# Kernel tuning notes

Measured on AMD Instinct MI355X. Metric: run time of the kernel, lower is better.

## Reference

```python
import jax, jax.numpy as jnp
from jax import lax
import numpy as np

RNN = 512; FC = 512; COND = 128; FEAT = 80; NCLS = 256; HALF = RNN // 2
PAD = 2; SCALES = (5, 5, 11); MEL_T = 86  # -> 22550 output samples


def setup_inputs() -> dict:
    key = jax.random.key(0)
    ks = jax.random.split(key, 12)
    s = 0.05
    p = {"mels": jax.random.normal(ks[0], (1, FEAT, MEL_T), jnp.float32)}
    ch = FEAT
    for i, sc in enumerate(SCALES):
        k = 2 * sc + 1
        p[f"up_w{i}"] = jax.random.normal(ks[1 + i], (COND, ch, k), jnp.float32) * s
        p[f"up_b{i}"] = jnp.zeros((COND,), jnp.float32)
        ch = COND
    p["Wx"] = jax.random.normal(ks[4], (3 * RNN, 3 + COND), jnp.float32) * s
    p["bx"] = jnp.zeros((3 * RNN,), jnp.float32)
    p["Wh"] = jax.random.normal(ks[5], (3 * RNN, RNN), jnp.float32) * s
    p["bh"] = jnp.zeros((3 * RNN,), jnp.float32)
    p["O1w"] = jax.random.normal(ks[6], (FC, HALF), jnp.float32) * s
    p["O1b"] = jnp.zeros((FC,), jnp.float32)
    p["O2w"] = jax.random.normal(ks[7], (NCLS, FC), jnp.float32) * s
    p["O2b"] = jnp.zeros((NCLS,), jnp.float32)
    p["O3w"] = jax.random.normal(ks[8], (FC, HALF), jnp.float32) * s
    p["O3b"] = jnp.zeros((FC,), jnp.float32)
    p["O4w"] = jax.random.normal(ks[9], (NCLS, FC), jnp.float32) * s
    p["O4b"] = jnp.zeros((NCLS,), jnp.float32)
    return p


def _upsample(mels, ws, bs):
    # mels[:, :, excess_pad:-excess_pad] with excess_pad = PAD - 1 = 1
    x = mels[:, :, PAD - 1:-(PAD - 1)]
    for w, b, sc in zip(ws, bs, SCALES):
        k = 2 * sc + 1
        # ConvTranspose1d(stride=sc, kernel=k, padding=(3*sc-1)//2) as an
        # input-dilated conv: edge pad = k-1-torch_pad = (sc+1)//2
        e = k - 1 - (3 * sc - 1) // 2
        x = lax.conv_general_dilated(x, w, window_strides=(1,),
                                     padding=[(e, e)], lhs_dilation=(sc,),
                                     dimension_numbers=('NCH', 'OIH', 'NCH'))
        x = jax.nn.relu(x + b[None, :, None])
    return x[0, :, 1:-1].T  # [T, COND]


def _gru(inp, h, Wx, bx, Wh, bh):
    xg = Wx @ inp + bx
    hg = Wh @ h + bh
    xr, xz, xn = jnp.split(xg, 3)
    hr, hz, hn = jnp.split(hg, 3)
    r = jax.nn.sigmoid(xr + hr)
    z = jax.nn.sigmoid(xz + hz)
    n = jnp.tanh(xn + r * hn)
    return (1.0 - z) * n + z * h


def reference(mels, up_w0, up_b0, up_w1, up_b1, up_w2, up_b2,
              Wx, bx, Wh, bh, O1w, O1b, O2w, O2b, O3w, O3b, O4w, O4b):
    cond = _upsample(mels, (up_w0, up_w1, up_w2), (up_b0, up_b1, up_b2))
    zero = jnp.float32(0.0)

    def step(carry, m_t):
        h, c_val, f_val = carry
        # coarse pass: x = [c_{t-1}, f_{t-1}, 0]
        inp1 = jnp.concatenate([jnp.stack([c_val, f_val, zero]), m_t])
        h1 = _gru(inp1, h, Wx, bx, Wh, bh)
        oc = O2w @ jax.nn.relu(O1w @ h1[:HALF] + O1b) + O2b
        c_cat = jnp.argmax(oc).astype(jnp.float32)  # deterministic=True path
        c_new = c_cat / 127.5 - 1.0
        # fine pass: x = [c_{t-1}, f_{t-1}, c_t]
        inp2 = jnp.concatenate([jnp.stack([c_val, f_val, c_new]), m_t])
        h2 = _gru(inp2, h, Wx, bx, Wh, bh)
        of = O4w @ jax.nn.relu(O3w @ h2[HALF:] + O3b) + O4b
        f_cat = jnp.argmax(of).astype(jnp.float32)
        f_new = f_cat / 127.5 - 1.0
        sample = (c_cat * 256.0 + f_cat) / 32767.5 - 1.0
        return (h2, c_new, f_new), (sample, jnp.concatenate([oc, of]))

    init = (jnp.zeros((RNN,), jnp.float32), zero, zero)
    _, (samples, logits) = lax.scan(step, init, cond)
    return samples, logits  # [T], [T, 512]
```

## Files before the change

### kernel.cpp

```cpp
#include <hip/hip_runtime.h>
#include <math.h>

#define T_STEPS 22550
#define NWG 32
#define NTHR 256

typedef unsigned long long ull;

#define SL_PRE  0
#define SL_PLC  2048
#define SL_PLF  10240
#define SL_END  18432

#define OF_SLOT  64
#define OF_AFTER (OF_SLOT + SL_END*2)
#define OF_BUFA  OF_AFTER
#define OF_BUFB  (OF_BUFA + 128*412)
#define OF_COND  (OF_BUFB + 128*2052)

__global__ void k_init(float* ws){
  int i = blockIdx.x*blockDim.x + threadIdx.x;
  ull* sl = (ull*)(ws + OF_SLOT);
  if (i < SL_END) __hip_atomic_store(&sl[i], 0ULL, __ATOMIC_RELAXED, __HIP_MEMORY_SCOPE_AGENT);
}

__global__ void k_upconv(const float* __restrict__ x, int instride, int inoff,
                         const float* __restrict__ w, const float* __restrict__ b,
                         float* __restrict__ y, int Cin, int Lin, int K, int sc, int e,
                         int Lout, int mode)
{
  int j = blockIdx.x*blockDim.x + threadIdx.x;
  int c = blockIdx.y;
  if (j >= Lout) return;
  float acc = b[c];
  int kstart = ((e - j) % sc + sc) % sc;
  for (int i = 0; i < Cin; ++i){
    const float* wci = w + (c*Cin + i)*K;
    const float* xi  = x + i*instride + inoff;
    for (int k = kstart; k < K; k += sc){
      int qd = j - e + k;
      if (qd >= 0){
        int qq = qd / sc;
        if (qq < Lin) acc += wci[k]*xi[qq];
      }
    }
  }
  acc = fmaxf(acc, 0.f);
  if (mode == 0) y[c*Lout + j] = acc;
  else { int t = j - 1; if (t >= 0 && t < T_STEPS) y[t*128 + c] = acc; }
}

__device__ __forceinline__ float sigm(float x){ return 1.f/(1.f + expf(-x)); }

__device__ __forceinline__ void pub64(ull* p, ull pk){
  (void)__hip_atomic_exchange(p, pk, __ATOMIC_RELAXED, __HIP_MEMORY_SCOPE_AGENT);
}
__device__ __forceinline__ ull ld64(ull* p){
  return __hip_atomic_load(p, __ATOMIC_RELAXED, __HIP_MEMORY_SCOPE_AGENT);
}
__device__ __forceinline__ ull pack_data(float v, unsigned tag){
  return ((ull)__float_as_uint(v) << 32) | (ull)tag;
}

__launch_bounds__(NTHR)
__global__ void k_wavernn(const float* __restrict__ Wx, const float* __restrict__ bx,
                          const float* __restrict__ Wh, const float* __restrict__ bh,
                          const float* __restrict__ O1w, const float* __restrict__ O1b,
                          const float* __restrict__ O2w, const float* __restrict__ O2b,
                          const float* __restrict__ O3w, const float* __restrict__ O3b,
                          const float* __restrict__ O4w, const float* __restrict__ O4b,
                          float* ws, float* __restrict__ out)
{
  __shared__ __align__(16) float h_s[512];
  __shared__ __align__(16) float m_s[128];
  __shared__ __align__(16) float h1_s[256];
  __shared__ __align__(16) float logit_s[256];
  __shared__ __align__(16) float pr_s[512], pz_s[512], pna_s[512], hn_s[512];
  __shared__ __align__(16) float w1r_s[512], w1z_s[512], w1n_s[512];
  __shared__ __align__(16) float w2r_s[512], w2z_s[512], w2n_s[512];
  __shared__ float o1own_s[16], o3own_s[16];
  __shared__ float hg_s[48], xgb_s[48];
  __shared__ float sc_s[8];
  __shared__ float wc0_s[48], bx_s[48], bh_s[48];

  const int tid = threadIdx.x, g = blockIdx.x;
  ull* sl = (ull*)(ws + OF_SLOT);
  const float* cond = ws + OF_COND;
  float* out_samp = out;
  float* out_log  = out + T_STEPS;

  if (tid < 48){
    int row = (tid>>4)*512 + g + 32*(tid&15);
    wc0_s[tid] = Wx[(size_t)row*131 + 0];
    bx_s[tid]  = bx[row];
    bh_s[tid]  = bh[row];
  }
  for (int e = tid; e < 512; e += NTHR){
    w1r_s[e] = Wx[(size_t)e*131 + 1];
    w1z_s[e] = Wx[(size_t)(512+e)*131 + 1];
    w1n_s[e] = Wx[(size_t)(1024+e)*131 + 1];
    w2r_s[e] = Wx[(size_t)e*131 + 2];
    w2z_s[e] = Wx[(size_t)(512+e)*131 + 2];
    w2n_s[e] = Wx[(size_t)(1024+e)*131 + 2];
  }
  const int m16 = tid>>4, c16 = tid&15;
  const int rowO1 = g + 32*m16;
  float wO1r[16], wO3r[16];
  #pragma unroll
  for (int k=0;k<16;++k){
    wO1r[k] = O1w[(size_t)rowO1*256 + c16*16 + k];
    wO3r[k] = O3w[(size_t)rowO1*256 + c16*16 + k];
  }
  const float bO1r = O1b[rowO1], bO3r = O3b[rowO1];
  float wPC[16], wPF[16];
  #pragma unroll
  for (int m=0;m<16;++m){
    wPC[m] = O2w[(size_t)tid*512 + g + 32*m];
    wPF[m] = O4w[(size_t)tid*512 + g + 32*m];
  }
  const float cbO2 = O2b[tid], cbO4 = O4b[tid];

  h_s[tid] = 0.f; h_s[tid+256] = 0.f;
  if (tid < 128) m_s[tid] = cond[tid];
  if (tid == 0){ sc_s[0] = 0.f; sc_s[2] = 0.f; sc_s[3] = 0.f; }
  __syncthreads();

  #define COMPUTE_WX() do { \
    if (tid < 192){ \
      const int li_ = tid>>2, q_ = tid&3; \
      const int row_ = (li_>>4)*512 + g + 32*(li_&15); \
      const float* WxR = Wx + (size_t)row_*131 + 3; \
      float aX = 0.f; \
      _Pragma("unroll") \
      for (int kk=0; kk<32; ++kk){ \
        int f_ = q_*32 + ((kk + 8*q_) & 31); \
        aX += WxR[f_]*m_s[f_]; \
      } \
      aX += __shfl_xor(aX,1); aX += __shfl_xor(aX,2); \
      if (q_ == 0) xgb_s[li_] = aX + bx_s[li_]; \
    } } while(0)

  #define COMPUTE_WH() do { \
    if (tid < 192){ \
      const int li_ = tid>>2, q_ = tid&3; \
      const int row_ = (li_>>4)*512 + g + 32*(li_&15); \
      const float4* W4 = (const float4*)(Wh + (size_t)row_*512); \
      const float4* H4 = (const float4*)h_s; \
      float aH = 0.f; \
      _Pragma("unroll") \
      for (int kk=0; kk<32; ++kk){ \
        int f_ = q_*32 + ((kk + 2*q_) & 31); \
        float4 w = W4[f_], v = H4[f_]; \
        aH += w.x*v.x + w.y*v.y + w.z*v.z + w.w*v.w; \
      } \
      aH += __shfl_xor(aH,1); aH += __shfl_xor(aH,2); \
      if (q_ == 0) hg_s[li_] = aH + bh_s[li_]; \
    } } while(0)

  #define PUB_PREGATES(TAGP) do { \
    if (tid < 64){ \
      const int i_ = tid>>2, c_ = tid&3; \
      const int e_ = g + 32*i_; \
      const float c0_ = sc_s[3]; \
      float v_; \
      if (c_ == 0)      v_ = xgb_s[i_]    + c0_*wc0_s[i_]    + hg_s[i_]; \
      else if (c_ == 1) v_ = xgb_s[16+i_] + c0_*wc0_s[16+i_] + hg_s[16+i_]; \
      else if (c_ == 2) v_ = xgb_s[32+i_] + c0_*wc0_s[32+i_]; \
      else              v_ = hg_s[32+i_]; \
      pub64(&sl[SL_PRE + e_*4 + c_], pack_data(v_, (TAGP))); \
    } } while(0)

  #define FAT_GATHER(BASE, BIAS) do { \
    ull pk_[32]; \
    _Pragma("unroll") \
    for (int g2=0; g2<32; ++g2) pk_[g2] = ld64(&sl[(BASE) + g2*256 + tid]); \
    for (;;){ \
      bool all_ = true; \
      _Pragma("unroll") \
      for (int g2=0; g2<32; ++g2) if ((unsigned)pk_[g2] != tag) all_ = false; \
      if (all_) break; \
      _Pragma("unroll") \
      for (int g2=0; g2<32; ++g2) \
        if ((unsigned)pk_[g2] != tag) pk_[g2] = ld64(&sl[(BASE) + g2*256 + tid]); \
    } \
    float s_ = (BIAS); \
    _Pragma("unroll") \
    for (int g2=0; g2<32; ++g2) s_ += __uint_as_float((unsigned)(pk_[g2] >> 32)); \
    logit_s[tid] = s_; \
  } while(0)

  COMPUTE_WX();
  if (tid < 48) hg_s[tid] = bh_s[tid];
  __syncthreads();
  PUB_PREGATES(1u);

  for (int t = 0; t < T_STEPS; ++t){
    const unsigned tag = (unsigned)(t + 1);

    {
      ull pk[8];
      #pragma unroll
      for (int c=0;c<4;++c){
        pk[c]   = ld64(&sl[SL_PRE + tid*4 + c]);
        pk[4+c] = ld64(&sl[SL_PRE + (tid+256)*4 + c]);
      }
      for (;;){
        bool all = true;
        #pragma unroll
        for (int i=0;i<8;++i) if ((unsigned)pk[i] != tag) all = false;
        if (all) break;
        #pragma unroll
        for (int i=0;i<8;++i)
          if ((unsigned)pk[i] != tag){
            int slot = (i<4) ? (tid*4 + i) : ((tid+256)*4 + (i-4));
            pk[i] = ld64(&sl[SL_PRE + slot]);
          }
      }
      pr_s[tid]      = __uint_as_float((unsigned)(pk[0] >> 32));
      pz_s[tid]      = __uint_as_float((unsigned)(pk[1] >> 32));
      pna_s[tid]     = __uint_as_float((unsigned)(pk[2] >> 32));
      hn_s[tid]      = __uint_as_float((unsigned)(pk[3] >> 32));
      pr_s[tid+256]  = __uint_as_float((unsigned)(pk[4] >> 32));
      pz_s[tid+256]  = __uint_as_float((unsigned)(pk[5] >> 32));
      pna_s[tid+256] = __uint_as_float((unsigned)(pk[6] >> 32));
      hn_s[tid+256]  = __uint_as_float((unsigned)(pk[7] >> 32));
    }
    if (tid < 128 && t + 1 < T_STEPS) m_s[tid] = cond[(size_t)(t+1)*128 + tid];
    __syncthreads();

    {
      const float f = sc_s[0];
      float r = sigm(pr_s[tid]  + f*w1r_s[tid]);
      float z = sigm(pz_s[tid]  + f*w1z_s[tid]);
      float n = tanhf(pna_s[tid] + f*w1n_s[tid] + r*hn_s[tid]);
      h1_s[tid] = (1.f - z)*n + z*h_s[tid];
    }
    __syncthreads();

    {
      float acc = 0.f;
      #pragma unroll
      for (int k=0;k<16;++k) acc += wO1r[k]*h1_s[c16*16 + k];
      acc += __shfl_xor(acc,1); acc += __shfl_xor(acc,2);
      acc += __shfl_xor(acc,4); acc += __shfl_xor(acc,8);
      if (c16 == 0) o1own_s[m16] = fmaxf(acc + bO1r, 0.f);
    }
    __syncthreads();
    {
      float s = 0.f;
      #pragma unroll
      for (int m=0;m<16;++m) s += wPC[m]*o1own_s[m];
      pub64(&sl[SL_PLC + g*256 + tid], pack_data(s, tag));
    }

    COMPUTE_WX();

    FAT_GATHER(SL_PLC, cbO2);
    __syncthreads();
    if (tid < 8) out_log[(size_t)t*512 + g*8 + tid] = logit_s[g*8 + tid];
    if (tid < 64){
      float bv = logit_s[tid]; int bi = tid;
      #pragma unroll
      for (int j=1;j<4;++j){ float v = logit_s[tid + 64*j]; if (v > bv){ bv = v; bi = tid + 64*j; } }
      #pragma unroll
      for (int off=32; off>=1; off>>=1){
        float ov = __shfl_xor(bv,off); int oi = __shfl_xor(bi,off);
        if (ov > bv || (ov == bv && oi < bi)){ bv = ov; bi = oi; }
      }
      if (tid == 0){ sc_s[2] = (float)bi; sc_s[3] = (float)bi/127.5f - 1.f; }
    }
    __syncthreads();

    {
      const float f = sc_s[0], cn = sc_s[3];
      #pragma unroll
      for (int hh=0; hh<2; ++hh){
        int e = tid + 256*hh;
        float r = sigm(pr_s[e]  + f*w1r_s[e] + cn*w2r_s[e]);
        float z = sigm(pz_s[e]  + f*w1z_s[e] + cn*w2z_s[e]);
        float n = tanhf(pna_s[e] + f*w1n_s[e] + cn*w2n_s[e] + r*hn_s[e]);
        h_s[e] = (1.f - z)*n + z*h_s[e];
      }
    }
    __syncthreads();

    {
      float acc = 0.f;
      #pragma unroll
      for (int k=0;k<16;++k) acc += wO3r[k]*h_s[256 + c16*16 + k];
      acc += __shfl_xor(acc,1); acc += __shfl_xor(acc,2);
      acc += __shfl_xor(acc,4); acc += __shfl_xor(acc,8);
      if (c16 == 0) o3own_s[m16] = fmaxf(acc + bO3r, 0.f);
    }
    __syncthreads();
    {
      float s = 0.f;
      #pragma unroll
      for (int m=0;m<16;++m) s += wPF[m]*o3own_s[m];
      pub64(&sl[SL_PLF + g*256 + tid], pack_data(s, tag));
    }

    COMPUTE_WH();
    __syncthreads();
    if (t + 1 < T_STEPS) PUB_PREGATES((unsigned)(t + 2));

    FAT_GATHER(SL_PLF, cbO4);
    __syncthreads();
    if (tid < 8) out_log[(size_t)t*512 + 256 + g*8 + tid] = logit_s[g*8 + tid];
    if (tid < 64){
      float bv = logit_s[tid]; int bi = tid;
      #pragma unroll
      for (int j=1;j<4;++j){ float v = logit_s[tid + 64*j]; if (v > bv){ bv = v; bi = tid + 64*j; } }
      #pragma unroll
      for (int off=32; off>=1; off>>=1){
        float ov = __shfl_xor(bv,off); int oi = __shfl_xor(bi,off);
        if (ov > bv || (ov == bv && oi < bi)){ bv = ov; bi = oi; }
      }
      if (tid == 0){
        sc_s[0] = (float)bi/127.5f - 1.f;
        if (g == 0) out_samp[t] = (sc_s[2]*256.f + (float)bi)/32767.5f - 1.f;
      }
    }
  }
}

extern "C" void kernel_launch(void* const* d_in, const int* in_sizes, int n_in,
                              void* d_out, int out_size, void* d_ws, size_t ws_size,
                              hipStream_t stream)
{
  const float* mels  = (const float*)d_in[0];
  const float* up_w0 = (const float*)d_in[1]; const float* up_b0 = (const float*)d_in[2];
  const float* up_w1 = (const float*)d_in[3]; const float* up_b1 = (const float*)d_in[4];
  const float* up_w2 = (const float*)d_in[5]; const float* up_b2 = (const float*)d_in[6];
  const float* Wx  = (const float*)d_in[7];  const float* bx  = (const float*)d_in[8];
  const float* Wh  = (const float*)d_in[9];  const float* bh  = (const float*)d_in[10];
  const float* O1w = (const float*)d_in[11]; const float* O1b = (const float*)d_in[12];
  const float* O2w = (const float*)d_in[13]; const float* O2b = (const float*)d_in[14];
  const float* O3w = (const float*)d_in[15]; const float* O3b = (const float*)d_in[16];
  const float* O4w = (const float*)d_in[17]; const float* O4b = (const float*)d_in[18];
  float* ws  = (float*)d_ws;
  float* out = (float*)d_out;

  k_init<<<(SL_END + 255)/256, 256, 0, stream>>>(ws);

  k_upconv<<<dim3((412  +127)/128, 128), 128, 0, stream>>>(mels,        86,   1, up_w0, up_b0,
            ws+OF_BUFA,  80,   84, 11,  5, 3,   412, 0);
  k_upconv<<<dim3((2052 +127)/128, 128), 128, 0, stream>>>(ws+OF_BUFA, 412,   0, up_w1, up_b1,
            ws+OF_BUFB, 128,  412, 11,  5, 3,  2052, 0);
  k_upconv<<<dim3((22552+127)/128, 128), 128, 0, stream>>>(ws+OF_BUFB, 2052,  0, up_w2, up_b2,
            ws+OF_COND, 128, 2052, 23, 11, 6, 22552, 1);

  k_wavernn<<<NWG, NTHR, 0, stream>>>(Wx, bx, Wh, bh, O1w, O1b, O2w, O2b,
                                      O3w, O3b, O4w, O4b, ws, out);
}
```

Baseline: 295.9 ms.

## Halve persistent workgroups to 16 with 512 threads each

Repartitions the persistent recurrent kernel from 32 workgroups of 256 threads to 16 workgroups of 512 threads. Each workgroup now owns twice as many GRU rows and output-layer columns, and the cross-workgroup logit gather reads 16 partial slots instead of 32, split over two thread halves and reduced in shared memory. The aim is to cut the cost of inter-workgroup flag polling and communication on every timestep. In exchange, each workgroup does more serial work per step, holds more weight registers, and adds an extra barrier inside the gather.

```diff
diff --git a/kernel.cpp b/kernel.cpp
--- a/kernel.cpp
+++ b/kernel.cpp
@@ -2,15 +2,15 @@
 #include <math.h>
 
 #define T_STEPS 22550
-#define NWG 32
-#define NTHR 256
+#define NWG 16
+#define NTHR 512
 
 typedef unsigned long long ull;
 
 #define SL_PRE  0
 #define SL_PLC  2048
-#define SL_PLF  10240
-#define SL_END  18432
+#define SL_PLF  6144
+#define SL_END  10240
 
 #define OF_SLOT  64
 #define OF_AFTER (OF_SLOT + SL_END*2)
@@ -75,13 +75,14 @@
   __shared__ __align__(16) float m_s[128];
   __shared__ __align__(16) float h1_s[256];
   __shared__ __align__(16) float logit_s[256];
+  __shared__ __align__(16) float part_s[512];
   __shared__ __align__(16) float pr_s[512], pz_s[512], pna_s[512], hn_s[512];
   __shared__ __align__(16) float w1r_s[512], w1z_s[512], w1n_s[512];
   __shared__ __align__(16) float w2r_s[512], w2z_s[512], w2n_s[512];
-  __shared__ float o1own_s[16], o3own_s[16];
-  __shared__ float hg_s[48], xgb_s[48];
+  __shared__ float o1own_s[32], o3own_s[32];
+  __shared__ float hg_s[96], xgb_s[96];
   __shared__ float sc_s[8];
-  __shared__ float wc0_s[48], bx_s[48], bh_s[48];
+  __shared__ float wc0_s[96], bx_s[96], bh_s[96];
 
   const int tid = threadIdx.x, g = blockIdx.x;
   ull* sl = (ull*)(ws + OF_SLOT);
@@ -89,13 +90,14 @@
   float* out_samp = out;
   float* out_log  = out + T_STEPS;
 
-  if (tid < 48){
-    int row = (tid>>4)*512 + g + 32*(tid&15);
+  if (tid < 96){
+    int row = (tid>>5)*512 + g + 16*(tid&31);
     wc0_s[tid] = Wx[(size_t)row*131 + 0];
     bx_s[tid]  = bx[row];
     bh_s[tid]  = bh[row];
   }
-  for (int e = tid; e < 512; e += NTHR){
+  if (tid < 512){
+    int e = tid;
     w1r_s[e] = Wx[(size_t)e*131 + 1];
     w1z_s[e] = Wx[(size_t)(512+e)*131 + 1];
     w1n_s[e] = Wx[(size_t)(1024+e)*131 + 1];
@@ -103,8 +105,8 @@
     w2z_s[e] = Wx[(size_t)(512+e)*131 + 2];
     w2n_s[e] = Wx[(size_t)(1024+e)*131 + 2];
   }
-  const int m16 = tid>>4, c16 = tid&15;
-  const int rowO1 = g + 32*m16;
+  const int m32 = tid>>4, c16 = tid&15;
+  const int rowO1 = g + 16*m32;
   float wO1r[16], wO3r[16];
   #pragma unroll
   for (int k=0;k<16;++k){
@@ -112,23 +114,26 @@
     wO3r[k] = O3w[(size_t)rowO1*256 + c16*16 + k];
   }
   const float bO1r = O1b[rowO1], bO3r = O3b[rowO1];
-  float wPC[16], wPF[16];
-  #pragma unroll
-  for (int m=0;m<16;++m){
-    wPC[m] = O2w[(size_t)tid*512 + g + 32*m];
-    wPF[m] = O4w[(size_t)tid*512 + g + 32*m];
-  }
-  const float cbO2 = O2b[tid], cbO4 = O4b[tid];
-
-  h_s[tid] = 0.f; h_s[tid+256] = 0.f;
+  float wPC[32], wPF[32];
+  float cbO2 = 0.f, cbO4 = 0.f;
+  if (tid < 256){
+    #pragma unroll
+    for (int m=0;m<32;++m){
+      wPC[m] = O2w[(size_t)tid*512 + g + 16*m];
+      wPF[m] = O4w[(size_t)tid*512 + g + 16*m];
+    }
+    cbO2 = O2b[tid]; cbO4 = O4b[tid];
+  }
+
+  h_s[tid] = 0.f;
   if (tid < 128) m_s[tid] = cond[tid];
   if (tid == 0){ sc_s[0] = 0.f; sc_s[2] = 0.f; sc_s[3] = 0.f; }
   __syncthreads();
 
   #define COMPUTE_WX() do { \
-    if (tid < 192){ \
+    if (tid < 384){ \
       const int li_ = tid>>2, q_ = tid&3; \
-      const int row_ = (li_>>4)*512 + g + 32*(li_&15); \
+      const int row_ = (li_>>5)*512 + g + 16*(li_&31); \
       const float* WxR = Wx + (size_t)row_*131 + 3; \
       float aX = 0.f; \
       _Pragma("unroll") \
@@ -141,9 +146,9 @@
     } } while(0)
 
   #define COMPUTE_WH() do { \
-    if (tid < 192){ \
+    if (tid < 384){ \
       const int li_ = tid>>2, q_ = tid&3; \
-      const int row_ = (li_>>4)*512 + g + 32*(li_&15); \
+      const int row_ = (li_>>5)*512 + g + 16*(li_&31); \
       const float4* W4 = (const float4*)(Wh + (size_t)row_*512); \
       const float4* H4 = (const float4*)h_s; \
       float aH = 0.f; \
@@ -158,39 +163,43 @@
     } } while(0)
 
   #define PUB_PREGATES(TAGP) do { \
-    if (tid < 64){ \
+    if (tid < 128){ \
       const int i_ = tid>>2, c_ = tid&3; \
-      const int e_ = g + 32*i_; \
+      const int e_ = g + 16*i_; \
       const float c0_ = sc_s[3]; \
       float v_; \
       if (c_ == 0)      v_ = xgb_s[i_]    + c0_*wc0_s[i_]    + hg_s[i_]; \
-      else if (c_ == 1) v_ = xgb_s[16+i_] + c0_*wc0_s[16+i_] + hg_s[16+i_]; \
-      else if (c_ == 2) v_ = xgb_s[32+i_] + c0_*wc0_s[32+i_]; \
-      else              v_ = hg_s[32+i_]; \
+      else if (c_ == 1) v_ = xgb_s[32+i_] + c0_*wc0_s[32+i_] + hg_s[32+i_]; \
+      else if (c_ == 2) v_ = xgb_s[64+i_] + c0_*wc0_s[64+i_]; \
+      else              v_ = hg_s[64+i_]; \
       pub64(&sl[SL_PRE + e_*4 + c_], pack_data(v_, (TAGP))); \
     } } while(0)
 
   #define FAT_GATHER(BASE, BIAS) do { \
-    ull pk_[32]; \
+    const int j_ = tid & 255, hh_ = tid >> 8; \
+    ull pk_[8]; \
     _Pragma("unroll") \
-    for (int g2=0; g2<32; ++g2) pk_[g2] = ld64(&sl[(BASE) + g2*256 + tid]); \
+    for (int g2=0; g2<8; ++g2) pk_[g2] = ld64(&sl[(BASE) + (hh_*8 + g2)*256 + j_]); \
     for (;;){ \
       bool all_ = true; \
       _Pragma("unroll") \
-      for (int g2=0; g2<32; ++g2) if ((unsigned)pk_[g2] != tag) all_ = false; \
+      for (int g2=0; g2<8; ++g2) if ((unsigned)pk_[g2] != tag) all_ = false; \
       if (all_) break; \
       _Pragma("unroll") \
-      for (int g2=0; g2<32; ++g2) \
-        if ((unsigned)pk_[g2] != tag) pk_[g2] = ld64(&sl[(BASE) + g2*256 + tid]); \
+      for (int g2=0; g2<8; ++g2) \
+        if ((unsigned)pk_[g2] != tag) pk_[g2] = ld64(&sl[(BASE) + (hh_*8 + g2)*256 + j_]); \
     } \
-    float s_ = (BIAS); \
+    float s_ = 0.f; \
     _Pragma("unroll") \
-    for (int g2=0; g2<32; ++g2) s_ += __uint_as_float((unsigned)(pk_[g2] >> 32)); \
-    logit_s[tid] = s_; \
+    for (int g2=0; g2<8; ++g2) s_ += __uint_as_float((unsigned)(pk_[g2] >> 32)); \
+    part_s[tid] = s_; \
+    __syncthreads(); \
+    if (tid < 256) logit_s[tid] = part_s[tid] + part_s[tid + 256] + (BIAS); \
+    __syncthreads(); \
   } while(0)
 
   COMPUTE_WX();
-  if (tid < 48) hg_s[tid] = bh_s[tid];
+  if (tid < 96) hg_s[tid] = bh_s[tid];
   __syncthreads();
   PUB_PREGATES(1u);
 
@@ -198,37 +207,27 @@
     const unsigned tag = (unsigned)(t + 1);
 
     {
-      ull pk[8];
-      #pragma unroll
-      for (int c=0;c<4;++c){
-        pk[c]   = ld64(&sl[SL_PRE + tid*4 + c]);
-        pk[4+c] = ld64(&sl[SL_PRE + (tid+256)*4 + c]);
-      }
+      ull pk[4];
+      #pragma unroll
+      for (int c=0;c<4;++c) pk[c] = ld64(&sl[SL_PRE + tid*4 + c]);
       for (;;){
         bool all = true;
         #pragma unroll
-        for (int i=0;i<8;++i) if ((unsigned)pk[i] != tag) all = false;
+        for (int i=0;i<4;++i) if ((unsigned)pk[i] != tag) all = false;
         if (all) break;
         #pragma unroll
-        for (int i=0;i<8;++i)
-          if ((unsigned)pk[i] != tag){
-            int slot = (i<4) ? (tid*4 + i) : ((tid+256)*4 + (i-4));
-            pk[i] = ld64(&sl[SL_PRE + slot]);
-          }
-      }
-      pr_s[tid]      = __uint_as_float((unsigned)(pk[0] >> 32));
-      pz_s[tid]      = __uint_as_float((unsigned)(pk[1] >> 32));
-      pna_s[tid]     = __uint_as_float((unsigned)(pk[2] >> 32));
-      hn_s[tid]      = __uint_as_float((unsigned)(pk[3] >> 32));
-      pr_s[tid+256]  = __uint_as_float((unsigned)(pk[4] >> 32));
-      pz_s[tid+256]  = __uint_as_float((unsigned)(pk[5] >> 32));
-      pna_s[tid+256] = __uint_as_float((unsigned)(pk[6] >> 32));
-      hn_s[tid+256]  = __uint_as_float((unsigned)(pk[7] >> 32));
+        for (int i=0;i<4;++i)
+          if ((unsigned)pk[i] != tag) pk[i] = ld64(&sl[SL_PRE + tid*4 + i]);
+      }
+      pr_s[tid]  = __uint_as_float((unsigned)(pk[0] >> 32));
+      pz_s[tid]  = __uint_as_float((unsigned)(pk[1] >> 32));
+      pna_s[tid] = __uint_as_float((unsigned)(pk[2] >> 32));
+      hn_s[tid]  = __uint_as_float((unsigned)(pk[3] >> 32));
     }
     if (tid < 128 && t + 1 < T_STEPS) m_s[tid] = cond[(size_t)(t+1)*128 + tid];
     __syncthreads();
 
-    {
+    if (tid < 256){
       const float f = sc_s[0];
       float r = sigm(pr_s[tid]  + f*w1r_s[tid]);
       float z = sigm(pz_s[tid]  + f*w1z_s[tid]);
@@ -243,21 +242,20 @@
       for (int k=0;k<16;++k) acc += wO1r[k]*h1_s[c16*16 + k];
       acc += __shfl_xor(acc,1); acc += __shfl_xor(acc,2);
       acc += __shfl_xor(acc,4); acc += __shfl_xor(acc,8);
-      if (c16 == 0) o1own_s[m16] = fmaxf(acc + bO1r, 0.f);
-    }
-    __syncthreads();
-    {
+      if (c16 == 0) o1own_s[m32] = fmaxf(acc + bO1r, 0.f);
+    }
+    __syncthreads();
+    if (tid < 256){
       float s = 0.f;
       #pragma unroll
-      for (int m=0;m<16;++m) s += wPC[m]*o1own_s[m];
+      for (int m=0;m<32;++m) s += wPC[m]*o1own_s[m];
       pub64(&sl[SL_PLC + g*256 + tid], pack_data(s, tag));
     }
 
     COMPUTE_WX();
 
     FAT_GATHER(SL_PLC, cbO2);
-    __syncthreads();
-    if (tid < 8) out_log[(size_t)t*512 + g*8 + tid] = logit_s[g*8 + tid];
+    if (tid < 16) out_log[(size_t)t*512 + g*16 + tid] = logit_s[g*16 + tid];
     if (tid < 64){
       float bv = logit_s[tid]; int bi = tid;
       #pragma unroll
@@ -273,14 +271,10 @@
 
     {
       const float f = sc_s[0], cn = sc_s[3];
-      #pragma unroll
-      for (int hh=0; hh<2; ++hh){
-        int e = tid + 256*hh;
-        float r = sigm(pr_s[e]  + f*w1r_s[e] + cn*w2r_s[e]);
-        float z = sigm(pz_s[e]  + f*w1z_s[e] + cn*w2z_s[e]);
-        float n = tanhf(pna_s[e] + f*w1n_s[e] + cn*w2n_s[e] + r*hn_s[e]);
-        h_s[e] = (1.f - z)*n + z*h_s[e];
-      }
+      float r = sigm(pr_s[tid]  + f*w1r_s[tid] + cn*w2r_s[tid]);
+      float z = sigm(pz_s[tid]  + f*w1z_s[tid] + cn*w2z_s[tid]);
+      float n = tanhf(pna_s[tid] + f*w1n_s[tid] + cn*w2n_s[tid] + r*hn_s[tid]);
+      h_s[tid] = (1.f - z)*n + z*h_s[tid];
     }
     __syncthreads();
 
@@ -290,13 +284,13 @@
       for (int k=0;k<16;++k) acc += wO3r[k]*h_s[256 + c16*16 + k];
       acc += __shfl_xor(acc,1); acc += __shfl_xor(acc,2);
       acc += __shfl_xor(acc,4); acc += __shfl_xor(acc,8);
-      if (c16 == 0) o3own_s[m16] = fmaxf(acc + bO3r, 0.f);
-    }
-    __syncthreads();
-    {
+      if (c16 == 0) o3own_s[m32] = fmaxf(acc + bO3r, 0.f);
+    }
+    __syncthreads();
+    if (tid < 256){
       float s = 0.f;
       #pragma unroll
-      for (int m=0;m<16;++m) s += wPF[m]*o3own_s[m];
+      for (int m=0;m<32;++m) s += wPF[m]*o3own_s[m];
       pub64(&sl[SL_PLF + g*256 + tid], pack_data(s, tag));
     }
 
@@ -305,8 +299,7 @@
     if (t + 1 < T_STEPS) PUB_PREGATES((unsigned)(t + 2));
 
     FAT_GATHER(SL_PLF, cbO4);
-    __syncthreads();
-    if (tid < 8) out_log[(size_t)t*512 + 256 + g*8 + tid] = logit_s[g*8 + tid];
+    if (tid < 16) out_log[(size_t)t*512 + 256 + g*16 + tid] = logit_s[g*16 + tid];
     if (tid < 64){
       float bv = logit_s[tid]; int bi = tid;
       #pragma unroll
```

New measurement: 381.8 ms. +29.0%, slower.
